# Kernel optimization log

Hardware: AMD Instinct MI355X
Metric: run time of the kernel (lower is better)

Reference implementation:

```python
import jax, jax.numpy as jnp
import numpy as np

H, KVH, D = 32, 8, 128            # query heads, kv heads, head dim
HIDDEN = H * D                     # 4096
B, S = 32, 2048                    # decode batch, max kv length
THETA = 10000.0
SCALE = D ** -0.5


def setup_inputs() -> dict:
    key = jax.random.key(0)
    ks = jax.random.split(key, 6)
    return {
        "hidden_states": jax.random.normal(ks[0], (B, HIDDEN), jnp.float32),
        "w_qkv": jax.random.normal(ks[1], ((H + 2 * KVH) * D, HIDDEN), jnp.float32) * (HIDDEN ** -0.5),
        "w_o": jax.random.normal(ks[2], (HIDDEN, HIDDEN), jnp.float32) * (HIDDEN ** -0.5),
        "k_cache": jax.random.normal(ks[3], (B, S, KVH, D), jnp.float32),
        "v_cache": jax.random.normal(ks[4], (B, S, KVH, D), jnp.float32),
        "positions": jax.random.randint(ks[5], (B,), 0, S, jnp.int32),
    }


def _rope(x, positions):
    # x: [B, nheads, D], neox-style rotary over full head dim
    half = D // 2
    inv_freq = 1.0 / (THETA ** (jnp.arange(0, half, dtype=jnp.float32) / half))
    freqs = positions.astype(jnp.float32)[:, None] * inv_freq[None, :]   # [B, half]
    cos = jnp.cos(freqs)[:, None, :]
    sin = jnp.sin(freqs)[:, None, :]
    x1, x2 = x[..., :half], x[..., half:]
    return jnp.concatenate([x1 * cos - x2 * sin, x2 * cos + x1 * sin], axis=-1)


def reference(hidden_states, w_qkv, w_o, k_cache, v_cache, positions):
    G = H // KVH  # query heads per kv head
    qkv = hidden_states @ w_qkv.T                      # [B, (H+2*KVH)*D]
    q, k, v = jnp.split(qkv, [H * D, (H + KVH) * D], axis=-1)
    q = _rope(q.reshape(B, H, D), positions)           # [B, H, D]
    k = _rope(k.reshape(B, KVH, D), positions)         # [B, KVH, D]
    v = v.reshape(B, KVH, D)

    # write current token's k/v into the cache at its position (paged-cache write)
    slot = (jnp.arange(S)[None, :] == positions[:, None])[:, :, None, None]  # [B,S,1,1]
    keys = jnp.where(slot, k[:, None], k_cache)        # [B, S, KVH, D]
    vals = jnp.where(slot, v[:, None], v_cache)

    qg = q.reshape(B, KVH, G, D)
    scores = jnp.einsum("bkgd,bskd->bkgs", qg, keys) * SCALE   # [B, KVH, G, S]
    valid = (jnp.arange(S)[None, :] <= positions[:, None])[:, None, None, :]
    scores = jnp.where(valid, scores, -jnp.inf)
    probs = jax.nn.softmax(scores, axis=-1)
    attn = jnp.einsum("bkgs,bskd->bkgd", probs, vals).reshape(B, H * D)
    return attn @ w_o.T                                # [B, HIDDEN]
```

## Files before the change

kernel.cpp:

```cpp
#include <hip/hip_runtime.h>
#include <hip/hip_bf16.h>

#define NH   32
#define NKVH 8
#define NG   4
#define DD   128
#define HID  4096
#define NQKV 6144
#define NB   32
#define SS   2048
#define SCALE 0.08838834764831845f
#define CHUNK 128
#define NCHUNK 16

typedef __attribute__((ext_vector_type(4))) float f32x4;
typedef __attribute__((ext_vector_type(8))) short bf16x8;

static __device__ __forceinline__ unsigned short f2bf(float f) {
    __hip_bfloat16 h = __float2bfloat16(f);
    return __builtin_bit_cast(unsigned short, h);
}

__global__ void cvt_hs(const float* __restrict__ in, unsigned short* __restrict__ out) {
    int i = blockIdx.x * 256 + threadIdx.x;
    out[i] = f2bf(in[i]);
}

template<int SPLIT>
__global__ __launch_bounds__(256) void gemm32_s(
    const unsigned short* __restrict__ Abf,
    const float* __restrict__ W,
    float* __restrict__ Part,
    int K, int N) {
    int j0 = blockIdx.x * 16;
    int ks = blockIdx.y;
    int tid = threadIdx.x;
    int wave = tid >> 6;
    int lane = tid & 63;
    int l16 = lane & 15;
    int kgrp = lane >> 4;
    int Kslice = K / SPLIT;
    int Kq = Kslice >> 2;
    int kbeg = ks * Kslice + wave * Kq;
    int kend = kbeg + Kq;

    f32x4 acc0 = {0.f, 0.f, 0.f, 0.f};
    f32x4 acc1 = {0.f, 0.f, 0.f, 0.f};
    const unsigned short* arow0 = Abf + (size_t)l16 * K;
    const unsigned short* arow1 = Abf + (size_t)(16 + l16) * K;
    const float* wrow = W + (size_t)(j0 + l16) * K;

#pragma unroll 2
    for (int k = kbeg; k < kend; k += 32) {
        int kk = k + kgrp * 8;
        bf16x8 a0 = *(const bf16x8*)(arow0 + kk);
        bf16x8 a1 = *(const bf16x8*)(arow1 + kk);
        f32x4 w0 = *(const f32x4*)(wrow + kk);
        f32x4 w1 = *(const f32x4*)(wrow + kk + 4);
        bf16x8 bw;
        bw[0] = (short)f2bf(w0[0]); bw[1] = (short)f2bf(w0[1]);
        bw[2] = (short)f2bf(w0[2]); bw[3] = (short)f2bf(w0[3]);
        bw[4] = (short)f2bf(w1[0]); bw[5] = (short)f2bf(w1[1]);
        bw[6] = (short)f2bf(w1[2]); bw[7] = (short)f2bf(w1[3]);
        acc0 = __builtin_amdgcn_mfma_f32_16x16x32_bf16(a0, bw, acc0, 0, 0, 0);
        acc1 = __builtin_amdgcn_mfma_f32_16x16x32_bf16(a1, bw, acc1, 0, 0, 0);
    }

    __shared__ f32x4 red[4][2][64];
    red[wave][0][lane] = acc0;
    red[wave][1][lane] = acc1;
    __syncthreads();
    if (wave == 0) {
        for (int t = 0; t < 2; ++t) {
            f32x4 s = red[0][t][lane];
            s += red[1][t][lane];
            s += red[2][t][lane];
            s += red[3][t][lane];
            for (int r = 0; r < 4; ++r)
                Part[((size_t)ks * 32 + t * 16 + kgrp * 4 + r) * N + j0 + l16] = s[r];
        }
    }
}

__global__ __launch_bounds__(256) void reduce_rope(
    const float* __restrict__ part, const int* __restrict__ positions,
    float* __restrict__ q_rope, float* __restrict__ k_rope, float* __restrict__ vbuf) {
    int idx = blockIdx.x * 256 + threadIdx.x;
    const int NROPE = NB * 40 * 64;
    const int NV = NB * NKVH * DD;
    if (idx < NROPE) {
        int i = idx & 63;
        int head = (idx >> 6) % 40;
        int b = idx / (64 * 40);
        size_t base = (size_t)b * NQKV + head * DD;
        float x1 = part[base + i] + part[(size_t)32 * NQKV + base + i];
        float x2 = part[base + i + 64] + part[(size_t)32 * NQKV + base + i + 64];
        float pos = (float)positions[b];
        float inv = exp2f(-(float)i * 0.20762050593046f);
        float f = pos * inv;
        float s, c;
        sincosf(f, &s, &c);
        float o1 = x1 * c - x2 * s;
        float o2 = x2 * c + x1 * s;
        if (head < NH) {
            float* dst = q_rope + ((size_t)b * NH + head) * DD;
            dst[i] = o1; dst[i + 64] = o2;
        } else {
            float* dst = k_rope + ((size_t)b * NKVH + (head - NH)) * DD;
            dst[i] = o1; dst[i + 64] = o2;
        }
    } else if (idx < NROPE + NV) {
        int j = idx - NROPE;
        size_t base = (size_t)(j >> 10) * NQKV + (NH + NKVH) * DD + (j & 1023);
        vbuf[j] = part[base] + part[(size_t)32 * NQKV + base];
    }
}

__global__ __launch_bounds__(256) void attn_partial(
    const float* __restrict__ k_cache, const float* __restrict__ v_cache,
    const float* __restrict__ q_rope, const float* __restrict__ k_rope,
    const float* __restrict__ vbuf, const int* __restrict__ positions,
    float* __restrict__ part) {
    int bk = blockIdx.x;
    int c = blockIdx.y;
    int b = bk >> 3, kvh = bk & 7;
    int pos = positions[b];
    int s0 = c * CHUNK;
    float* mypart = part + ((size_t)bk * NCHUNK + c) * 520;
    int tid = threadIdx.x;
    if (s0 > pos) {
        if (tid < 4) { mypart[tid] = -__builtin_inff(); mypart[4 + tid] = 0.f; }
        return;
    }
    int nvalid = min(pos + 1 - s0, CHUNK);

    __shared__ float sc[4][CHUNK];
    __shared__ float mg[4], lg[4];
    __shared__ f32x4 red[8][4][32];

    for (int i = tid; i < 4 * CHUNK; i += 256) ((float*)sc)[i] = -__builtin_inff();
    __syncthreads();

    int wave = tid >> 6, lane = tid & 63, l16 = lane & 15, rsub = lane >> 4;

    float qf[4][8];
    const float* qbase = q_rope + ((size_t)b * NH + kvh * NG) * DD;
#pragma unroll
    for (int g = 0; g < 4; ++g)
#pragma unroll
        for (int e = 0; e < 8; ++e)
            qf[g][e] = qbase[g * DD + l16 * 8 + e];

    for (int it = 0; it < CHUNK / 16; ++it) {
        int row = it * 16 + wave * 4 + rsub;
        if (row >= nvalid) continue;
        int s = s0 + row;
        const float* krow = (s == pos)
            ? (k_rope + ((size_t)b * NKVH + kvh) * DD)
            : (k_cache + (((size_t)b * SS + s) * NKVH + kvh) * DD);
        f32x4 k0 = *(const f32x4*)(krow + l16 * 8);
        f32x4 k1 = *(const f32x4*)(krow + l16 * 8 + 4);
        float dots[4];
#pragma unroll
        for (int g = 0; g < 4; ++g) {
            dots[g] = qf[g][0] * k0[0] + qf[g][1] * k0[1] + qf[g][2] * k0[2] + qf[g][3] * k0[3]
                    + qf[g][4] * k1[0] + qf[g][5] * k1[1] + qf[g][6] * k1[2] + qf[g][7] * k1[3];
        }
#pragma unroll
        for (int m = 1; m < 16; m <<= 1)
#pragma unroll
            for (int g = 0; g < 4; ++g)
                dots[g] += __shfl_xor(dots[g], m, 64);
        if (l16 == 0)
#pragma unroll
            for (int g = 0; g < 4; ++g) sc[g][row] = dots[g] * SCALE;
    }
    __syncthreads();

    {
        int g = wave;
        float v0 = sc[g][lane], v1 = sc[g][lane + 64];
        float m = fmaxf(v0, v1);
#pragma unroll
        for (int msk = 1; msk < 64; msk <<= 1) m = fmaxf(m, __shfl_xor(m, msk, 64));
        float p0 = expf(v0 - m), p1 = expf(v1 - m);
        float l = p0 + p1;
#pragma unroll
        for (int msk = 1; msk < 64; msk <<= 1) l += __shfl_xor(l, msk, 64);
        sc[g][lane] = p0; sc[g][lane + 64] = p1;
        if (lane == 0) { mg[g] = m; lg[g] = l; }
    }
    __syncthreads();

    int sid = tid >> 5, l32 = tid & 31;
    f32x4 acc[4] = {{0.f,0.f,0.f,0.f},{0.f,0.f,0.f,0.f},{0.f,0.f,0.f,0.f},{0.f,0.f,0.f,0.f}};
    for (int row = sid; row < nvalid; row += 8) {
        int s = s0 + row;
        const float* vrow = (s == pos)
            ? (vbuf + ((size_t)b * NKVH + kvh) * DD)
            : (v_cache + (((size_t)b * SS + s) * NKVH + kvh) * DD);
        f32x4 v4 = *(const f32x4*)(vrow + l32 * 4);
#pragma unroll
        for (int g = 0; g < 4; ++g)
            acc[g] += sc[g][row] * v4;
    }
#pragma unroll
    for (int g = 0; g < 4; ++g) red[sid][g][l32] = acc[g];
    __syncthreads();

    if (tid < 128) {
        int g = tid >> 5, l = tid & 31;
        f32x4 s = red[0][g][l];
#pragma unroll
        for (int w = 1; w < 8; ++w) s += red[w][g][l];
        *(f32x4*)(mypart + 8 + g * DD + l * 4) = s;
        if (l == 0) { mypart[g] = mg[g]; mypart[4 + g] = lg[g]; }
    }
}

__global__ __launch_bounds__(128) void attn_combine(
    const float* __restrict__ part, unsigned short* __restrict__ attn_bf) {
    int bk = blockIdx.x;
    int b = bk >> 3, kvh = bk & 7;
    const float* p0 = part + (size_t)bk * NCHUNK * 520;
    int tid = threadIdx.x;
    int g = tid >> 5, l32 = tid & 31;

    float M = -__builtin_inff();
#pragma unroll
    for (int c = 0; c < NCHUNK; ++c) {
        float lcv = p0[c * 520 + 4 + g];
        float mcv = p0[c * 520 + g];
        if (lcv > 0.f && mcv > M) M = mcv;
    }
    float L = 0.f;
    f32x4 acc = {0.f, 0.f, 0.f, 0.f};
#pragma unroll
    for (int c = 0; c < NCHUNK; ++c) {
        float lcv = p0[c * 520 + 4 + g];
        float mcv = p0[c * 520 + g];
        if (lcv > 0.f) {
            float wgt = expf(mcv - M);
            L += lcv * wgt;
            f32x4 a = *(const f32x4*)(p0 + c * 520 + 8 + g * DD + l32 * 4);
            acc += wgt * a;
        }
    }
    float inv = 1.0f / L;
    unsigned short* o = attn_bf + (((size_t)b * NH) + kvh * NG + g) * DD + l32 * 4;
#pragma unroll
    for (int r = 0; r < 4; ++r) o[r] = f2bf(acc[r] * inv);
}

__global__ __launch_bounds__(256) void reduce_o(const float* __restrict__ part,
                                                float* __restrict__ out) {
    int idx = blockIdx.x * 256 + threadIdx.x;
    const f32x4* p = (const f32x4*)part;
    f32x4 s = p[idx];
    s += p[idx + 32768];
    s += p[idx + 65536];
    s += p[idx + 98304];
    ((f32x4*)out)[idx] = s;
}

extern "C" void kernel_launch(void* const* d_in, const int* in_sizes, int n_in,
                              void* d_out, int out_size, void* d_ws, size_t ws_size,
                              hipStream_t stream) {
    const float* hs      = (const float*)d_in[0];
    const float* w_qkv   = (const float*)d_in[1];
    const float* w_o     = (const float*)d_in[2];
    const float* k_cache = (const float*)d_in[3];
    const float* v_cache = (const float*)d_in[4];
    const int*   positions = (const int*)d_in[5];
    float* out = (float*)d_out;

    char* ws = (char*)d_ws;
    unsigned short* hs_bf   = (unsigned short*)(ws);
    float* qkv_part         = (float*)(ws + 262144);
    float* q_rope           = (float*)(ws + 1835008);
    float* k_rope           = (float*)(ws + 2359296);
    float* vbuf             = (float*)(ws + 2490368);
    float* part             = (float*)(ws + 2621440);
    unsigned short* attn_bf = (unsigned short*)(ws + 11141120);
    float* o_part           = (float*)(ws + 11403264);

    hipLaunchKernelGGL(cvt_hs, dim3(512), dim3(256), 0, stream, hs, hs_bf);
    hipLaunchKernelGGL((gemm32_s<2>), dim3(NQKV / 16, 2), dim3(256), 0, stream,
                       hs_bf, w_qkv, qkv_part, HID, NQKV);
    hipLaunchKernelGGL(reduce_rope, dim3(448), dim3(256), 0, stream,
                       qkv_part, positions, q_rope, k_rope, vbuf);
    hipLaunchKernelGGL(attn_partial, dim3(NB * NKVH, NCHUNK), dim3(256), 0, stream,
                       k_cache, v_cache, q_rope, k_rope, vbuf, positions, part);
    hipLaunchKernelGGL(attn_combine, dim3(NB * NKVH), dim3(128), 0, stream, part, attn_bf);
    hipLaunchKernelGGL((gemm32_s<4>), dim3(HID / 16, 4), dim3(256), 0, stream,
                       attn_bf, w_o, o_part, HID, HID);
    hipLaunchKernelGGL(reduce_o, dim3(128), dim3(256), 0, stream, o_part, out);
}
```

Measured before the change: 130.9 us.

## Fuse QKV split-K reduction and RoPE into attention kernel, cheaper bf16 packing

```diff
diff --git a/kernel.cpp b/kernel.cpp
--- a/kernel.cpp
+++ b/kernel.cpp
@@ -15,10 +15,17 @@
 
 typedef __attribute__((ext_vector_type(4))) float f32x4;
 typedef __attribute__((ext_vector_type(8))) short bf16x8;
+typedef __attribute__((ext_vector_type(4))) unsigned int u32x4;
 
 static __device__ __forceinline__ unsigned short f2bf(float f) {
     __hip_bfloat16 h = __float2bfloat16(f);
     return __builtin_bit_cast(unsigned short, h);
+}
+
+static __device__ __forceinline__ unsigned int pack_bf16(float a, float b) {
+    unsigned int ua = __builtin_bit_cast(unsigned int, a) + 0x8000u;
+    unsigned int ub = __builtin_bit_cast(unsigned int, b) + 0x8000u;
+    return __builtin_amdgcn_perm(ub, ua, 0x07060302u);
 }
 
 __global__ void cvt_hs(const float* __restrict__ in, unsigned short* __restrict__ out) {
@@ -50,18 +57,19 @@
     const unsigned short* arow1 = Abf + (size_t)(16 + l16) * K;
     const float* wrow = W + (size_t)(j0 + l16) * K;
 
-#pragma unroll 2
+#pragma unroll 4
     for (int k = kbeg; k < kend; k += 32) {
         int kk = k + kgrp * 8;
         bf16x8 a0 = *(const bf16x8*)(arow0 + kk);
         bf16x8 a1 = *(const bf16x8*)(arow1 + kk);
         f32x4 w0 = *(const f32x4*)(wrow + kk);
         f32x4 w1 = *(const f32x4*)(wrow + kk + 4);
-        bf16x8 bw;
-        bw[0] = (short)f2bf(w0[0]); bw[1] = (short)f2bf(w0[1]);
-        bw[2] = (short)f2bf(w0[2]); bw[3] = (short)f2bf(w0[3]);
-        bw[4] = (short)f2bf(w1[0]); bw[5] = (short)f2bf(w1[1]);
-        bw[6] = (short)f2bf(w1[2]); bw[7] = (short)f2bf(w1[3]);
+        u32x4 pk;
+        pk[0] = pack_bf16(w0[0], w0[1]);
+        pk[1] = pack_bf16(w0[2], w0[3]);
+        pk[2] = pack_bf16(w1[0], w1[1]);
+        pk[3] = pack_bf16(w1[2], w1[3]);
+        bf16x8 bw = __builtin_bit_cast(bf16x8, pk);
         acc0 = __builtin_amdgcn_mfma_f32_16x16x32_bf16(a0, bw, acc0, 0, 0, 0);
         acc1 = __builtin_amdgcn_mfma_f32_16x16x32_bf16(a1, bw, acc1, 0, 0, 0);
     }
@@ -82,44 +90,9 @@
     }
 }
 
-__global__ __launch_bounds__(256) void reduce_rope(
-    const float* __restrict__ part, const int* __restrict__ positions,
-    float* __restrict__ q_rope, float* __restrict__ k_rope, float* __restrict__ vbuf) {
-    int idx = blockIdx.x * 256 + threadIdx.x;
-    const int NROPE = NB * 40 * 64;
-    const int NV = NB * NKVH * DD;
-    if (idx < NROPE) {
-        int i = idx & 63;
-        int head = (idx >> 6) % 40;
-        int b = idx / (64 * 40);
-        size_t base = (size_t)b * NQKV + head * DD;
-        float x1 = part[base + i] + part[(size_t)32 * NQKV + base + i];
-        float x2 = part[base + i + 64] + part[(size_t)32 * NQKV + base + i + 64];
-        float pos = (float)positions[b];
-        float inv = exp2f(-(float)i * 0.20762050593046f);
-        float f = pos * inv;
-        float s, c;
-        sincosf(f, &s, &c);
-        float o1 = x1 * c - x2 * s;
-        float o2 = x2 * c + x1 * s;
-        if (head < NH) {
-            float* dst = q_rope + ((size_t)b * NH + head) * DD;
-            dst[i] = o1; dst[i + 64] = o2;
-        } else {
-            float* dst = k_rope + ((size_t)b * NKVH + (head - NH)) * DD;
-            dst[i] = o1; dst[i + 64] = o2;
-        }
-    } else if (idx < NROPE + NV) {
-        int j = idx - NROPE;
-        size_t base = (size_t)(j >> 10) * NQKV + (NH + NKVH) * DD + (j & 1023);
-        vbuf[j] = part[base] + part[(size_t)32 * NQKV + base];
-    }
-}
-
 __global__ __launch_bounds__(256) void attn_partial(
     const float* __restrict__ k_cache, const float* __restrict__ v_cache,
-    const float* __restrict__ q_rope, const float* __restrict__ k_rope,
-    const float* __restrict__ vbuf, const int* __restrict__ positions,
+    const float* __restrict__ qkv_part, const int* __restrict__ positions,
     float* __restrict__ part) {
     int bk = blockIdx.x;
     int c = blockIdx.y;
@@ -134,32 +107,62 @@
     }
     int nvalid = min(pos + 1 - s0, CHUNK);
 
+    __shared__ __attribute__((aligned(16))) float raw[768];
+    __shared__ float cs0[64], sn0[64];
     __shared__ float sc[4][CHUNK];
     __shared__ float mg[4], lg[4];
     __shared__ f32x4 red[8][4][32];
 
     for (int i = tid; i < 4 * CHUNK; i += 256) ((float*)sc)[i] = -__builtin_inff();
+    if (tid < 64) {
+        float inv = exp2f(-(float)tid * 0.20762050593046f);
+        float f = (float)pos * inv;
+        sincosf(f, &sn0[tid], &cs0[tid]);
+    }
+    for (int idx = tid; idx < 768; idx += 256) {
+        int col;
+        if (idx < 512)      col = (kvh * NG) * DD + idx;
+        else if (idx < 640) col = (NH + kvh) * DD + (idx - 512);
+        else                col = (NH + NKVH + kvh) * DD + (idx - 640);
+        size_t base = (size_t)b * NQKV + col;
+        raw[idx] = qkv_part[base]
+                 + qkv_part[base + (size_t)32 * NQKV]
+                 + qkv_part[base + (size_t)64 * NQKV]
+                 + qkv_part[base + (size_t)96 * NQKV];
+    }
+    __syncthreads();
+    for (int idx = tid; idx < 320; idx += 256) {
+        int h = idx >> 6, i = idx & 63;
+        int off = h * 128;
+        float x1 = raw[off + i], x2 = raw[off + i + 64];
+        float c0 = cs0[i], s1 = sn0[i];
+        raw[off + i] = x1 * c0 - x2 * s1;
+        raw[off + i + 64] = x2 * c0 + x1 * s1;
+    }
     __syncthreads();
 
     int wave = tid >> 6, lane = tid & 63, l16 = lane & 15, rsub = lane >> 4;
 
     float qf[4][8];
-    const float* qbase = q_rope + ((size_t)b * NH + kvh * NG) * DD;
 #pragma unroll
     for (int g = 0; g < 4; ++g)
 #pragma unroll
         for (int e = 0; e < 8; ++e)
-            qf[g][e] = qbase[g * DD + l16 * 8 + e];
+            qf[g][e] = raw[g * DD + l16 * 8 + e];
 
     for (int it = 0; it < CHUNK / 16; ++it) {
         int row = it * 16 + wave * 4 + rsub;
         if (row >= nvalid) continue;
         int s = s0 + row;
-        const float* krow = (s == pos)
-            ? (k_rope + ((size_t)b * NKVH + kvh) * DD)
-            : (k_cache + (((size_t)b * SS + s) * NKVH + kvh) * DD);
-        f32x4 k0 = *(const f32x4*)(krow + l16 * 8);
-        f32x4 k1 = *(const f32x4*)(krow + l16 * 8 + 4);
+        f32x4 k0, k1;
+        if (s == pos) {
+            k0 = *(const f32x4*)(&raw[512 + l16 * 8]);
+            k1 = *(const f32x4*)(&raw[512 + l16 * 8 + 4]);
+        } else {
+            const float* krow = k_cache + (((size_t)b * SS + s) * NKVH + kvh) * DD;
+            k0 = *(const f32x4*)(krow + l16 * 8);
+            k1 = *(const f32x4*)(krow + l16 * 8 + 4);
+        }
         float dots[4];
 #pragma unroll
         for (int g = 0; g < 4; ++g) {
@@ -196,10 +199,13 @@
     f32x4 acc[4] = {{0.f,0.f,0.f,0.f},{0.f,0.f,0.f,0.f},{0.f,0.f,0.f,0.f},{0.f,0.f,0.f,0.f}};
     for (int row = sid; row < nvalid; row += 8) {
         int s = s0 + row;
-        const float* vrow = (s == pos)
-            ? (vbuf + ((size_t)b * NKVH + kvh) * DD)
-            : (v_cache + (((size_t)b * SS + s) * NKVH + kvh) * DD);
-        f32x4 v4 = *(const f32x4*)(vrow + l32 * 4);
+        f32x4 v4;
+        if (s == pos) {
+            v4 = *(const f32x4*)(&raw[640 + l32 * 4]);
+        } else {
+            const float* vrow = v_cache + (((size_t)b * SS + s) * NKVH + kvh) * DD;
+            v4 = *(const f32x4*)(vrow + l32 * 4);
+        }
 #pragma unroll
         for (int g = 0; g < 4; ++g)
             acc[g] += sc[g][row] * v4;
@@ -277,20 +283,15 @@
     char* ws = (char*)d_ws;
     unsigned short* hs_bf   = (unsigned short*)(ws);
     float* qkv_part         = (float*)(ws + 262144);
-    float* q_rope           = (float*)(ws + 1835008);
-    float* k_rope           = (float*)(ws + 2359296);
-    float* vbuf             = (float*)(ws + 2490368);
-    float* part             = (float*)(ws + 2621440);
-    unsigned short* attn_bf = (unsigned short*)(ws + 11141120);
-    float* o_part           = (float*)(ws + 11403264);
+    float* part             = (float*)(ws + 3407872);
+    unsigned short* attn_bf = (unsigned short*)(ws + 11927552);
+    float* o_part           = (float*)(ws + 12189696);
 
     hipLaunchKernelGGL(cvt_hs, dim3(512), dim3(256), 0, stream, hs, hs_bf);
-    hipLaunchKernelGGL((gemm32_s<2>), dim3(NQKV / 16, 2), dim3(256), 0, stream,
+    hipLaunchKernelGGL((gemm32_s<4>), dim3(NQKV / 16, 4), dim3(256), 0, stream,
                        hs_bf, w_qkv, qkv_part, HID, NQKV);
-    hipLaunchKernelGGL(reduce_rope, dim3(448), dim3(256), 0, stream,
-                       qkv_part, positions, q_rope, k_rope, vbuf);
     hipLaunchKernelGGL(attn_partial, dim3(NB * NKVH, NCHUNK), dim3(256), 0, stream,
-                       k_cache, v_cache, q_rope, k_rope, vbuf, positions, part);
+                       k_cache, v_cache, qkv_part, positions, part);
     hipLaunchKernelGGL(attn_combine, dim3(NB * NKVH), dim3(128), 0, stream, part, attn_bf);
     hipLaunchKernelGGL((gemm32_s<4>), dim3(HID / 16, 4), dim3(256), 0, stream,
                        attn_bf, w_o, o_part, HID, HID);
```

Measured after the change: 131.0 us. Within noise of the previous version (+0.1%).

## Fuse attention decode pipeline into one cooperative persistent kernel with grid syncs

Applied to the files above, without the earlier changes.

```diff
diff --git a/kernel.cpp b/kernel.cpp
--- a/kernel.cpp
+++ b/kernel.cpp
@@ -1,5 +1,8 @@
 #include <hip/hip_runtime.h>
 #include <hip/hip_bf16.h>
+#include <hip/hip_cooperative_groups.h>
+
+namespace cg = cooperative_groups;
 
 #define NH   32
 #define NKVH 8
@@ -12,136 +15,172 @@
 #define SCALE 0.08838834764831845f
 #define CHUNK 128
 #define NCHUNK 16
+#define QSPLIT 8
+#define OSPLIT 8
 
 typedef __attribute__((ext_vector_type(4))) float f32x4;
 typedef __attribute__((ext_vector_type(8))) short bf16x8;
+typedef __attribute__((ext_vector_type(4))) unsigned int u32x4;
+
+#define OFF_QKVP  0u
+#define OFF_QR    1572864u
+#define OFF_KR    1703936u
+#define OFF_VB    1736704u
+#define OFF_PART  1769472u
+#define OFF_ABF   3899392u
+#define OFF_OPART 3964928u
+#define OFF_CNT   5013504u
 
 static __device__ __forceinline__ unsigned short f2bf(float f) {
     __hip_bfloat16 h = __float2bfloat16(f);
     return __builtin_bit_cast(unsigned short, h);
 }
 
-__global__ void cvt_hs(const float* __restrict__ in, unsigned short* __restrict__ out) {
-    int i = blockIdx.x * 256 + threadIdx.x;
-    out[i] = f2bf(in[i]);
-}
-
-template<int SPLIT>
-__global__ __launch_bounds__(256) void gemm32_s(
-    const unsigned short* __restrict__ Abf,
-    const float* __restrict__ W,
-    float* __restrict__ Part,
-    int K, int N) {
-    int j0 = blockIdx.x * 16;
-    int ks = blockIdx.y;
-    int tid = threadIdx.x;
-    int wave = tid >> 6;
-    int lane = tid & 63;
-    int l16 = lane & 15;
-    int kgrp = lane >> 4;
-    int Kslice = K / SPLIT;
-    int Kq = Kslice >> 2;
-    int kbeg = ks * Kslice + wave * Kq;
-    int kend = kbeg + Kq;
-
-    f32x4 acc0 = {0.f, 0.f, 0.f, 0.f};
-    f32x4 acc1 = {0.f, 0.f, 0.f, 0.f};
-    const unsigned short* arow0 = Abf + (size_t)l16 * K;
-    const unsigned short* arow1 = Abf + (size_t)(16 + l16) * K;
-    const float* wrow = W + (size_t)(j0 + l16) * K;
-
-#pragma unroll 2
-    for (int k = kbeg; k < kend; k += 32) {
+static __device__ __forceinline__ unsigned int pack_bf16(float a, float b) {
+    unsigned int ua = __builtin_bit_cast(unsigned int, a) + 0x8000u;
+    unsigned int ub = __builtin_bit_cast(unsigned int, b) + 0x8000u;
+    return __builtin_amdgcn_perm(ub, ua, 0x07060302u);
+}
+
+
+static __device__ __forceinline__ void qkv_gemm_job(
+    int job, int wave, int lane, int l16, int kgrp,
+    const float* __restrict__ hs, const float* __restrict__ w_qkv,
+    float* __restrict__ qkv_part, f32x4 (*redsm)[2][64]) {
+    int jt = job % 384, ks = job / 384;
+    int j0 = jt * 16;
+    const int K = HID, Kslice = HID / QSPLIT;
+    int kbeg = ks * Kslice + wave * (Kslice / 4);
+    f32x4 acc0 = {0.f,0.f,0.f,0.f}, acc1 = {0.f,0.f,0.f,0.f};
+    const float* ar0 = hs + (size_t)l16 * K;
+    const float* ar1 = hs + (size_t)(16 + l16) * K;
+    const float* wr  = w_qkv + (size_t)(j0 + l16) * K;
+#pragma unroll
+    for (int k = kbeg; k < kbeg + Kslice / 4; k += 32) {
         int kk = k + kgrp * 8;
-        bf16x8 a0 = *(const bf16x8*)(arow0 + kk);
-        bf16x8 a1 = *(const bf16x8*)(arow1 + kk);
-        f32x4 w0 = *(const f32x4*)(wrow + kk);
-        f32x4 w1 = *(const f32x4*)(wrow + kk + 4);
-        bf16x8 bw;
-        bw[0] = (short)f2bf(w0[0]); bw[1] = (short)f2bf(w0[1]);
-        bw[2] = (short)f2bf(w0[2]); bw[3] = (short)f2bf(w0[3]);
-        bw[4] = (short)f2bf(w1[0]); bw[5] = (short)f2bf(w1[1]);
-        bw[6] = (short)f2bf(w1[2]); bw[7] = (short)f2bf(w1[3]);
+        f32x4 a00 = *(const f32x4*)(ar0 + kk), a01 = *(const f32x4*)(ar0 + kk + 4);
+        f32x4 a10 = *(const f32x4*)(ar1 + kk), a11 = *(const f32x4*)(ar1 + kk + 4);
+        f32x4 w0  = *(const f32x4*)(wr  + kk), w1  = *(const f32x4*)(wr  + kk + 4);
+        u32x4 pa0, pa1, pw;
+        pa0[0] = pack_bf16(a00[0], a00[1]); pa0[1] = pack_bf16(a00[2], a00[3]);
+        pa0[2] = pack_bf16(a01[0], a01[1]); pa0[3] = pack_bf16(a01[2], a01[3]);
+        pa1[0] = pack_bf16(a10[0], a10[1]); pa1[1] = pack_bf16(a10[2], a10[3]);
+        pa1[2] = pack_bf16(a11[0], a11[1]); pa1[3] = pack_bf16(a11[2], a11[3]);
+        pw[0]  = pack_bf16(w0[0],  w0[1]);  pw[1]  = pack_bf16(w0[2],  w0[3]);
+        pw[2]  = pack_bf16(w1[0],  w1[1]);  pw[3]  = pack_bf16(w1[2],  w1[3]);
+        bf16x8 bw = __builtin_bit_cast(bf16x8, pw);
+        acc0 = __builtin_amdgcn_mfma_f32_16x16x32_bf16(__builtin_bit_cast(bf16x8, pa0), bw, acc0, 0, 0, 0);
+        acc1 = __builtin_amdgcn_mfma_f32_16x16x32_bf16(__builtin_bit_cast(bf16x8, pa1), bw, acc1, 0, 0, 0);
+    }
+    redsm[wave][0][lane] = acc0;
+    redsm[wave][1][lane] = acc1;
+    __syncthreads();
+    if (wave == 0) {
+        for (int t = 0; t < 2; ++t) {
+            f32x4 s = redsm[0][t][lane];
+            s += redsm[1][t][lane]; s += redsm[2][t][lane]; s += redsm[3][t][lane];
+            for (int r = 0; r < 4; ++r)
+                qkv_part[((size_t)ks * 32 + t * 16 + kgrp * 4 + r) * NQKV + j0 + l16] = s[r];
+        }
+    }
+    __syncthreads();
+}
+
+static __device__ __forceinline__ void o_gemm_job(
+    int job, int wave, int lane, int l16, int kgrp,
+    const unsigned short* __restrict__ attn_bf, const float* __restrict__ w_o,
+    float* __restrict__ o_part, f32x4 (*redsm)[2][64]) {
+    int jt = job & 255, ks = job >> 8;
+    int j0 = jt * 16;
+    const int K = HID, Kslice = HID / OSPLIT;
+    int kbeg = ks * Kslice + wave * (Kslice / 4);
+    f32x4 acc0 = {0.f,0.f,0.f,0.f}, acc1 = {0.f,0.f,0.f,0.f};
+    const unsigned short* ar0 = attn_bf + (size_t)l16 * K;
+    const unsigned short* ar1 = attn_bf + (size_t)(16 + l16) * K;
+    const float* wr = w_o + (size_t)(j0 + l16) * K;
+#pragma unroll
+    for (int k = kbeg; k < kbeg + Kslice / 4; k += 32) {
+        int kk = k + kgrp * 8;
+        bf16x8 a0 = *(const bf16x8*)(ar0 + kk);
+        bf16x8 a1 = *(const bf16x8*)(ar1 + kk);
+        f32x4 w0 = *(const f32x4*)(wr + kk), w1 = *(const f32x4*)(wr + kk + 4);
+        u32x4 pw;
+        pw[0] = pack_bf16(w0[0], w0[1]); pw[1] = pack_bf16(w0[2], w0[3]);
+        pw[2] = pack_bf16(w1[0], w1[1]); pw[3] = pack_bf16(w1[2], w1[3]);
+        bf16x8 bw = __builtin_bit_cast(bf16x8, pw);
         acc0 = __builtin_amdgcn_mfma_f32_16x16x32_bf16(a0, bw, acc0, 0, 0, 0);
         acc1 = __builtin_amdgcn_mfma_f32_16x16x32_bf16(a1, bw, acc1, 0, 0, 0);
     }
-
-    __shared__ f32x4 red[4][2][64];
-    red[wave][0][lane] = acc0;
-    red[wave][1][lane] = acc1;
+    redsm[wave][0][lane] = acc0;
+    redsm[wave][1][lane] = acc1;
     __syncthreads();
     if (wave == 0) {
         for (int t = 0; t < 2; ++t) {
-            f32x4 s = red[0][t][lane];
-            s += red[1][t][lane];
-            s += red[2][t][lane];
-            s += red[3][t][lane];
+            f32x4 s = redsm[0][t][lane];
+            s += redsm[1][t][lane]; s += redsm[2][t][lane]; s += redsm[3][t][lane];
             for (int r = 0; r < 4; ++r)
-                Part[((size_t)ks * 32 + t * 16 + kgrp * 4 + r) * N + j0 + l16] = s[r];
-        }
-    }
-}
-
-__global__ __launch_bounds__(256) void reduce_rope(
-    const float* __restrict__ part, const int* __restrict__ positions,
+                o_part[((size_t)ks * 32 + t * 16 + kgrp * 4 + r) * HID + j0 + l16] = s[r];
+        }
+    }
+    __syncthreads();
+}
+
+static __device__ __forceinline__ void rope_elem(
+    int idx, const float* __restrict__ qkv_part, const int* __restrict__ positions,
     float* __restrict__ q_rope, float* __restrict__ k_rope, float* __restrict__ vbuf) {
-    int idx = blockIdx.x * 256 + threadIdx.x;
     const int NROPE = NB * 40 * 64;
-    const int NV = NB * NKVH * DD;
     if (idx < NROPE) {
-        int i = idx & 63;
-        int head = (idx >> 6) % 40;
-        int b = idx / (64 * 40);
+        int i = idx & 63, head = (idx >> 6) % 40, b = idx / (64 * 40);
         size_t base = (size_t)b * NQKV + head * DD;
-        float x1 = part[base + i] + part[(size_t)32 * NQKV + base + i];
-        float x2 = part[base + i + 64] + part[(size_t)32 * NQKV + base + i + 64];
+        float x1 = 0.f, x2 = 0.f;
+#pragma unroll
+        for (int p = 0; p < QSPLIT; ++p) {
+            x1 += qkv_part[(size_t)p * 32 * NQKV + base + i];
+            x2 += qkv_part[(size_t)p * 32 * NQKV + base + i + 64];
+        }
         float pos = (float)positions[b];
         float inv = exp2f(-(float)i * 0.20762050593046f);
-        float f = pos * inv;
-        float s, c;
-        sincosf(f, &s, &c);
-        float o1 = x1 * c - x2 * s;
-        float o2 = x2 * c + x1 * s;
+        float fr = pos * inv, s, c;
+        sincosf(fr, &s, &c);
+        float o1 = x1 * c - x2 * s, o2 = x2 * c + x1 * s;
         if (head < NH) {
-            float* dst = q_rope + ((size_t)b * NH + head) * DD;
-            dst[i] = o1; dst[i + 64] = o2;
+            float* d = q_rope + ((size_t)b * NH + head) * DD;
+            d[i] = o1; d[i + 64] = o2;
         } else {
-            float* dst = k_rope + ((size_t)b * NKVH + (head - NH)) * DD;
-            dst[i] = o1; dst[i + 64] = o2;
-        }
-    } else if (idx < NROPE + NV) {
+            float* d = k_rope + ((size_t)b * NKVH + (head - NH)) * DD;
+            d[i] = o1; d[i + 64] = o2;
+        }
+    } else {
         int j = idx - NROPE;
         size_t base = (size_t)(j >> 10) * NQKV + (NH + NKVH) * DD + (j & 1023);
-        vbuf[j] = part[base] + part[(size_t)32 * NQKV + base];
-    }
-}
-
-__global__ __launch_bounds__(256) void attn_partial(
+        float v = 0.f;
+#pragma unroll
+        for (int p = 0; p < QSPLIT; ++p) v += qkv_part[(size_t)p * 32 * NQKV + base];
+        vbuf[j] = v;
+    }
+}
+
+static __device__ __forceinline__ void attn_job(
+    int job, int tid, int wave, int lane, int l16,
     const float* __restrict__ k_cache, const float* __restrict__ v_cache,
     const float* __restrict__ q_rope, const float* __restrict__ k_rope,
     const float* __restrict__ vbuf, const int* __restrict__ positions,
-    float* __restrict__ part) {
-    int bk = blockIdx.x;
-    int c = blockIdx.y;
+    float* __restrict__ part,
+    float (*sc)[CHUNK], float* mg, float* lg, f32x4 (*red2)[4][32]) {
+    int bk = job & 255, c = job >> 8;
     int b = bk >> 3, kvh = bk & 7;
     int pos = positions[b];
     int s0 = c * CHUNK;
     float* mypart = part + ((size_t)bk * NCHUNK + c) * 520;
-    int tid = threadIdx.x;
     if (s0 > pos) {
         if (tid < 4) { mypart[tid] = -__builtin_inff(); mypart[4 + tid] = 0.f; }
         return;
     }
     int nvalid = min(pos + 1 - s0, CHUNK);
-
-    __shared__ float sc[4][CHUNK];
-    __shared__ float mg[4], lg[4];
-    __shared__ f32x4 red[8][4][32];
+    int rsub = lane >> 4;
 
     for (int i = tid; i < 4 * CHUNK; i += 256) ((float*)sc)[i] = -__builtin_inff();
     __syncthreads();
-
-    int wave = tid >> 6, lane = tid & 63, l16 = lane & 15, rsub = lane >> 4;
 
     float qf[4][8];
     const float* qbase = q_rope + ((size_t)b * NH + kvh * NG) * DD;
@@ -151,29 +190,54 @@
         for (int e = 0; e < 8; ++e)
             qf[g][e] = qbase[g * DD + l16 * 8 + e];
 
-    for (int it = 0; it < CHUNK / 16; ++it) {
-        int row = it * 16 + wave * 4 + rsub;
-        if (row >= nvalid) continue;
-        int s = s0 + row;
-        const float* krow = (s == pos)
-            ? (k_rope + ((size_t)b * NKVH + kvh) * DD)
-            : (k_cache + (((size_t)b * SS + s) * NKVH + kvh) * DD);
-        f32x4 k0 = *(const f32x4*)(krow + l16 * 8);
-        f32x4 k1 = *(const f32x4*)(krow + l16 * 8 + 4);
-        float dots[4];
-#pragma unroll
-        for (int g = 0; g < 4; ++g) {
-            dots[g] = qf[g][0] * k0[0] + qf[g][1] * k0[1] + qf[g][2] * k0[2] + qf[g][3] * k0[3]
-                    + qf[g][4] * k1[0] + qf[g][5] * k1[1] + qf[g][6] * k1[2] + qf[g][7] * k1[3];
-        }
-#pragma unroll
-        for (int m = 1; m < 16; m <<= 1)
+    const float* kcb = k_cache + ((size_t)b * SS * NKVH + kvh) * DD;
+    const float* krp = k_rope + ((size_t)b * NKVH + kvh) * DD;
+
+    if (nvalid == CHUNK) {
+#pragma unroll
+        for (int it = 0; it < CHUNK / 16; ++it) {
+            int row = it * 16 + wave * 4 + rsub;
+            int s = s0 + row;
+            const float* krow = (s == pos) ? krp : (kcb + (size_t)s * (NKVH * DD));
+            f32x4 k0 = *(const f32x4*)(krow + l16 * 8);
+            f32x4 k1 = *(const f32x4*)(krow + l16 * 8 + 4);
+            float dots[4];
 #pragma unroll
             for (int g = 0; g < 4; ++g)
-                dots[g] += __shfl_xor(dots[g], m, 64);
-        if (l16 == 0)
-#pragma unroll
-            for (int g = 0; g < 4; ++g) sc[g][row] = dots[g] * SCALE;
+                dots[g] = qf[g][0]*k0[0] + qf[g][1]*k0[1] + qf[g][2]*k0[2] + qf[g][3]*k0[3]
+                        + qf[g][4]*k1[0] + qf[g][5]*k1[1] + qf[g][6]*k1[2] + qf[g][7]*k1[3];
+#pragma unroll
+            for (int m = 1; m < 16; m <<= 1)
+#pragma unroll
+                for (int g = 0; g < 4; ++g)
+                    dots[g] += __shfl_xor(dots[g], m, 64);
+            if (l16 == 0)
+#pragma unroll
+                for (int g = 0; g < 4; ++g) sc[g][row] = dots[g] * SCALE;
+        }
+    } else {
+#pragma unroll 2
+        for (int it = 0; it < CHUNK / 16; ++it) {
+            int row = it * 16 + wave * 4 + rsub;
+            if (row >= nvalid) continue;
+            int s = s0 + row;
+            const float* krow = (s == pos) ? krp : (kcb + (size_t)s * (NKVH * DD));
+            f32x4 k0 = *(const f32x4*)(krow + l16 * 8);
+            f32x4 k1 = *(const f32x4*)(krow + l16 * 8 + 4);
+            float dots[4];
+#pragma unroll
+            for (int g = 0; g < 4; ++g)
+                dots[g] = qf[g][0]*k0[0] + qf[g][1]*k0[1] + qf[g][2]*k0[2] + qf[g][3]*k0[3]
+                        + qf[g][4]*k1[0] + qf[g][5]*k1[1] + qf[g][6]*k1[2] + qf[g][7]*k1[3];
+#pragma unroll
+            for (int m = 1; m < 16; m <<= 1)
+#pragma unroll
+                for (int g = 0; g < 4; ++g)
+                    dots[g] += __shfl_xor(dots[g], m, 64);
+            if (l16 == 0)
+#pragma unroll
+                for (int g = 0; g < 4; ++g) sc[g][row] = dots[g] * SCALE;
+        }
     }
     __syncthreads();
 
@@ -194,38 +258,45 @@
 
     int sid = tid >> 5, l32 = tid & 31;
     f32x4 acc[4] = {{0.f,0.f,0.f,0.f},{0.f,0.f,0.f,0.f},{0.f,0.f,0.f,0.f},{0.f,0.f,0.f,0.f}};
-    for (int row = sid; row < nvalid; row += 8) {
-        int s = s0 + row;
-        const float* vrow = (s == pos)
-            ? (vbuf + ((size_t)b * NKVH + kvh) * DD)
-            : (v_cache + (((size_t)b * SS + s) * NKVH + kvh) * DD);
-        f32x4 v4 = *(const f32x4*)(vrow + l32 * 4);
-#pragma unroll
-        for (int g = 0; g < 4; ++g)
-            acc[g] += sc[g][row] * v4;
-    }
-#pragma unroll
-    for (int g = 0; g < 4; ++g) red[sid][g][l32] = acc[g];
-    __syncthreads();
-
+    const float* vcb = v_cache + ((size_t)b * SS * NKVH + kvh) * DD;
+    const float* vrp = vbuf + ((size_t)b * NKVH + kvh) * DD;
+    if (nvalid == CHUNK) {
+#pragma unroll 4
+        for (int row = sid; row < CHUNK; row += 8) {
+            int s = s0 + row;
+            const float* vrow = (s == pos) ? vrp : (vcb + (size_t)s * (NKVH * DD));
+            f32x4 v4 = *(const f32x4*)(vrow + l32 * 4);
+#pragma unroll
+            for (int g = 0; g < 4; ++g) acc[g] += sc[g][row] * v4;
+        }
+    } else {
+#pragma unroll 2
+        for (int row = sid; row < nvalid; row += 8) {
+            int s = s0 + row;
+            const float* vrow = (s == pos) ? vrp : (vcb + (size_t)s * (NKVH * DD));
+            f32x4 v4 = *(const f32x4*)(vrow + l32 * 4);
+#pragma unroll
+            for (int g = 0; g < 4; ++g) acc[g] += sc[g][row] * v4;
+        }
+    }
+#pragma unroll
+    for (int g = 0; g < 4; ++g) red2[sid][g][l32] = acc[g];
+    __syncthreads();
     if (tid < 128) {
         int g = tid >> 5, l = tid & 31;
-        f32x4 s = red[0][g][l];
-#pragma unroll
-        for (int w = 1; w < 8; ++w) s += red[w][g][l];
+        f32x4 s = red2[0][g][l];
+#pragma unroll
+        for (int w = 1; w < 8; ++w) s += red2[w][g][l];
         *(f32x4*)(mypart + 8 + g * DD + l * 4) = s;
         if (l == 0) { mypart[g] = mg[g]; mypart[4 + g] = lg[g]; }
     }
 }
 
-__global__ __launch_bounds__(128) void attn_combine(
-    const float* __restrict__ part, unsigned short* __restrict__ attn_bf) {
-    int bk = blockIdx.x;
+static __device__ __forceinline__ void combine_job(
+    int bk, int tid, const float* __restrict__ part, unsigned short* __restrict__ attn_bf) {
     int b = bk >> 3, kvh = bk & 7;
     const float* p0 = part + (size_t)bk * NCHUNK * 520;
-    int tid = threadIdx.x;
     int g = tid >> 5, l32 = tid & 31;
-
     float M = -__builtin_inff();
 #pragma unroll
     for (int c = 0; c < NCHUNK; ++c) {
@@ -252,15 +323,126 @@
     for (int r = 0; r < 4; ++r) o[r] = f2bf(acc[r] * inv);
 }
 
-__global__ __launch_bounds__(256) void reduce_o(const float* __restrict__ part,
-                                                float* __restrict__ out) {
+static __device__ __forceinline__ void reduce_o_elem(
+    int idx, const float* __restrict__ o_part, float* __restrict__ out) {
+    const f32x4* p = (const f32x4*)o_part;
+    f32x4 s = p[idx];
+#pragma unroll
+    for (int k = 1; k < OSPLIT; ++k) s += p[idx + k * 32768];
+    ((f32x4*)out)[idx] = s;
+}
+
+__global__ __launch_bounds__(256) void mega(
+    const float* __restrict__ hs, const float* __restrict__ w_qkv,
+    const float* __restrict__ w_o, const float* __restrict__ k_cache,
+    const float* __restrict__ v_cache, const int* __restrict__ positions,
+    float* __restrict__ out, float* __restrict__ wsf)
+{
+    cg::grid_group grid = cg::this_grid();
+    const int bid = blockIdx.x, tid = threadIdx.x;
+    const int wave = tid >> 6, lane = tid & 63, l16 = lane & 15, kgrp = lane >> 4;
+    const int nb = gridDim.x;
+
+    float* qkv_part = wsf + OFF_QKVP;
+    float* q_rope   = wsf + OFF_QR;
+    float* k_rope   = wsf + OFF_KR;
+    float* vbuf     = wsf + OFF_VB;
+    float* part     = wsf + OFF_PART;
+    unsigned short* attn_bf = (unsigned short*)(wsf + OFF_ABF);
+    float* o_part   = wsf + OFF_OPART;
+    unsigned int* cnt = (unsigned int*)(wsf + OFF_CNT);
+
+    __shared__ f32x4 redsm[4][2][64];
+    __shared__ float sc[4][CHUNK];
+    __shared__ float mg[4], lg[4];
+    __shared__ f32x4 red2[8][4][32];
+    __shared__ int jobsm;
+
+    if (bid == 0 && tid == 0) *cnt = 0u;
+
+    for (int job = bid; job < 384 * QSPLIT; job += nb)
+        qkv_gemm_job(job, wave, lane, l16, kgrp, hs, w_qkv, qkv_part, redsm);
+    __threadfence();
+    grid.sync();
+
+    for (int idx = bid * 256 + tid; idx < NB * 40 * 64 + NB * NKVH * DD; idx += nb * 256)
+        rope_elem(idx, qkv_part, positions, q_rope, k_rope, vbuf);
+    __threadfence();
+    grid.sync();
+
+    for (;;) {
+        __syncthreads();
+        if (tid == 0) jobsm = (int)atomicAdd(cnt, 1u);
+        __syncthreads();
+        int job = jobsm;
+        if (job >= NB * NKVH * NCHUNK) break;
+        attn_job(job, tid, wave, lane, l16, k_cache, v_cache, q_rope, k_rope,
+                 vbuf, positions, part, sc, mg, lg, red2);
+    }
+    __threadfence();
+    grid.sync();
+
+    for (int bk = bid; bk < NB * NKVH; bk += nb)
+        if (tid < 128) combine_job(bk, tid, part, attn_bf);
+    __threadfence();
+    grid.sync();
+
+    for (int job = bid; job < 256 * OSPLIT; job += nb)
+        o_gemm_job(job, wave, lane, l16, kgrp, attn_bf, w_o, o_part, redsm);
+    __threadfence();
+    grid.sync();
+
+    for (int idx = bid * 256 + tid; idx < 32768; idx += nb * 256)
+        reduce_o_elem(idx, o_part, out);
+}
+
+__global__ __launch_bounds__(256) void fb_qkv_gemm(
+    const float* __restrict__ hs, const float* __restrict__ w_qkv,
+    float* __restrict__ qkv_part) {
+    __shared__ f32x4 redsm[4][2][64];
+    int tid = threadIdx.x;
+    qkv_gemm_job(blockIdx.x + 384 * blockIdx.y, tid >> 6, tid & 63, tid & 15,
+                 (tid & 63) >> 4, hs, w_qkv, qkv_part, redsm);
+}
+
+__global__ __launch_bounds__(256) void fb_rope(
+    const float* __restrict__ qkv_part, const int* __restrict__ positions,
+    float* __restrict__ q_rope, float* __restrict__ k_rope, float* __restrict__ vbuf) {
     int idx = blockIdx.x * 256 + threadIdx.x;
-    const f32x4* p = (const f32x4*)part;
-    f32x4 s = p[idx];
-    s += p[idx + 32768];
-    s += p[idx + 65536];
-    s += p[idx + 98304];
-    ((f32x4*)out)[idx] = s;
+    if (idx < NB * 40 * 64 + NB * NKVH * DD)
+        rope_elem(idx, qkv_part, positions, q_rope, k_rope, vbuf);
+}
+
+__global__ __launch_bounds__(256) void fb_attn(
+    const float* __restrict__ k_cache, const float* __restrict__ v_cache,
+    const float* __restrict__ q_rope, const float* __restrict__ k_rope,
+    const float* __restrict__ vbuf, const int* __restrict__ positions,
+    float* __restrict__ part) {
+    __shared__ float sc[4][CHUNK];
+    __shared__ float mg[4], lg[4];
+    __shared__ f32x4 red2[8][4][32];
+    int tid = threadIdx.x;
+    attn_job(blockIdx.x + 256 * blockIdx.y, tid, tid >> 6, tid & 63, tid & 15,
+             k_cache, v_cache, q_rope, k_rope, vbuf, positions, part, sc, mg, lg, red2);
+}
+
+__global__ __launch_bounds__(128) void fb_combine(
+    const float* __restrict__ part, unsigned short* __restrict__ attn_bf) {
+    combine_job(blockIdx.x, threadIdx.x, part, attn_bf);
+}
+
+__global__ __launch_bounds__(256) void fb_o_gemm(
+    const unsigned short* __restrict__ attn_bf, const float* __restrict__ w_o,
+    float* __restrict__ o_part) {
+    __shared__ f32x4 redsm[4][2][64];
+    int tid = threadIdx.x;
+    o_gemm_job(blockIdx.x + 256 * blockIdx.y, tid >> 6, tid & 63, tid & 15,
+               (tid & 63) >> 4, attn_bf, w_o, o_part, redsm);
+}
+
+__global__ __launch_bounds__(256) void fb_reduce_o(
+    const float* __restrict__ o_part, float* __restrict__ out) {
+    reduce_o_elem(blockIdx.x * 256 + threadIdx.x, o_part, out);
 }
 
 extern "C" void kernel_launch(void* const* d_in, const int* in_sizes, int n_in,
@@ -273,26 +455,41 @@
     const float* v_cache = (const float*)d_in[4];
     const int*   positions = (const int*)d_in[5];
     float* out = (float*)d_out;
-
-    char* ws = (char*)d_ws;
-    unsigned short* hs_bf   = (unsigned short*)(ws);
-    float* qkv_part         = (float*)(ws + 262144);
-    float* q_rope           = (float*)(ws + 1835008);
-    float* k_rope           = (float*)(ws + 2359296);
-    float* vbuf             = (float*)(ws + 2490368);
-    float* part             = (float*)(ws + 2621440);
-    unsigned short* attn_bf = (unsigned short*)(ws + 11141120);
-    float* o_part           = (float*)(ws + 11403264);
-
-    hipLaunchKernelGGL(cvt_hs, dim3(512), dim3(256), 0, stream, hs, hs_bf);
-    hipLaunchKernelGGL((gemm32_s<2>), dim3(NQKV / 16, 2), dim3(256), 0, stream,
-                       hs_bf, w_qkv, qkv_part, HID, NQKV);
-    hipLaunchKernelGGL(reduce_rope, dim3(448), dim3(256), 0, stream,
-                       qkv_part, positions, q_rope, k_rope, vbuf);
-    hipLaunchKernelGGL(attn_partial, dim3(NB * NKVH, NCHUNK), dim3(256), 0, stream,
-                       k_cache, v_cache, q_rope, k_rope, vbuf, positions, part);
-    hipLaunchKernelGGL(attn_combine, dim3(NB * NKVH), dim3(128), 0, stream, part, attn_bf);
-    hipLaunchKernelGGL((gemm32_s<4>), dim3(HID / 16, 4), dim3(256), 0, stream,
-                       attn_bf, w_o, o_part, HID, HID);
-    hipLaunchKernelGGL(reduce_o, dim3(128), dim3(256), 0, stream, o_part, out);
-}
+    float* wsf = (float*)d_ws;
+
+    float* p_qkv_part = wsf + OFF_QKVP;
+    float* p_q_rope   = wsf + OFF_QR;
+    float* p_k_rope   = wsf + OFF_KR;
+    float* p_vbuf     = wsf + OFF_VB;
+    float* p_part     = wsf + OFF_PART;
+    unsigned short* p_attn_bf = (unsigned short*)(wsf + OFF_ABF);
+    float* p_o_part   = wsf + OFF_OPART;
+
+    int maxb = 0;
+    hipError_t qe = hipOccupancyMaxActiveBlocksPerMultiprocessor(
+        &maxb, (const void*)mega, 256, 0);
+    hipError_t le = hipErrorUnknown;
+    if (qe == hipSuccess && maxb > 0) {
+        int nblk = maxb * 256;
+        if (nblk > 1024) nblk = 1024;
+        const float* a0 = hs; const float* a1 = w_qkv; const float* a2 = w_o;
+        const float* a3 = k_cache; const float* a4 = v_cache;
+        const int* a5 = positions; float* a6 = out; float* a7 = wsf;
+        void* args[8] = { &a0, &a1, &a2, &a3, &a4, &a5, &a6, &a7 };
+        le = hipLaunchCooperativeKernel((const void*)mega, dim3(nblk), dim3(256),
+                                        args, 0, stream);
+    }
+    if (le != hipSuccess) {
+        (void)hipGetLastError();
+        hipLaunchKernelGGL(fb_qkv_gemm, dim3(384, QSPLIT), dim3(256), 0, stream,
+                           hs, w_qkv, p_qkv_part);
+        hipLaunchKernelGGL(fb_rope, dim3(448), dim3(256), 0, stream,
+                           p_qkv_part, positions, p_q_rope, p_k_rope, p_vbuf);
+        hipLaunchKernelGGL(fb_attn, dim3(256, NCHUNK), dim3(256), 0, stream,
+                           k_cache, v_cache, p_q_rope, p_k_rope, p_vbuf, positions, p_part);
+        hipLaunchKernelGGL(fb_combine, dim3(NB * NKVH), dim3(128), 0, stream, p_part, p_attn_bf);
+        hipLaunchKernelGGL(fb_o_gemm, dim3(256, OSPLIT), dim3(256), 0, stream,
+                           p_attn_bf, w_o, p_o_part);
+        hipLaunchKernelGGL(fb_reduce_o, dim3(128), dim3(256), 0, stream, p_o_part, out);
+    }
+}
```

Result: slower. 472.4 us (+260.8%).
